# Kernel optimization log

Hardware: AMD Instinct MI355X
Metric: run time of the kernel (lower is better)

## Reference

```python
import jax, jax.numpy as jnp
import numpy as np

N, D_IN, D_OUT, N_CTRS, K = 16384, 64, 64, 512, 16


def setup_inputs() -> dict:
    key = jax.random.key(0)
    k1, k2, k3, k4 = jax.random.split(key, 4)
    x = jax.random.normal(k1, (N, D_IN), dtype=jnp.float32)
    ctrs = jax.random.normal(k2, (N_CTRS, D_IN), dtype=jnp.float32)
    Wv = jax.random.normal(k3, (N_CTRS, D_IN, D_OUT), dtype=jnp.float32) * 0.02
    Ov = jax.random.normal(k4, (N_CTRS, D_OUT), dtype=jnp.float32) * 0.02
    return {"x": x, "ctrs": ctrs, "Wv": Wv, "Ov": Ov, "k": K}


def reference(x, ctrs, Wv, Ov, k):
    n = x.shape[0]
    # squared distances via expansion (same math as sum((x-c)^2), avoids [n,C,d] blowup)
    x2 = jnp.sum(x * x, axis=1, keepdims=True)            # [n,1]
    c2 = jnp.sum(ctrs * ctrs, axis=1)                     # [C]
    dist_sq = x2 + c2[None, :] - 2.0 * (x @ ctrs.T)       # [n,C]
    # k nearest centers; softmax over negative squared distances of the k selected
    neg_top, idx = jax.lax.top_k(-dist_sq, k)             # [n,k] each
    scores = jax.nn.softmax(neg_top, axis=1)              # [n,k]
    # dense soft-assignment matrix (only k nonzeros per row), as in the torch code
    A = jnp.zeros_like(dist_sq).at[jnp.arange(n)[:, None], idx].set(scores)  # [n,C]
    # per-token affine mix: sum_c A[n,c] * (x[n] @ Wv[c] + Ov[c])
    scored_weights = jnp.einsum('nc,cgp->ngp', A, Wv)     # [n,d_in,d_out]
    out = jnp.einsum('ngp,ng->np', scored_weights, x) + A @ Ov  # [n,d_out]
    return out
```

## Files before the change

kernel.cpp:

```cpp
#include <hip/hip_runtime.h>
#include <hip/hip_fp16.h>

#define N_TOK 16384
#define D 64
#define NC 512
#define KSEL 16
#define NPAIR (N_TOK * KSEL)
#define PADCAP 327168

typedef __attribute__((ext_vector_type(8))) short short8;
typedef __attribute__((ext_vector_type(8))) unsigned short ushort8;
typedef __attribute__((ext_vector_type(16))) float float16;

__device__ __forceinline__ unsigned fkey(float f) {
    unsigned u = __float_as_uint(f);
    return (u & 0x80000000u) ? ~u : (u | 0x80000000u);
}
__device__ __forceinline__ float funkey(unsigned k) {
    unsigned u = (k & 0x80000000u) ? (k & 0x7fffffffu) : ~k;
    return __uint_as_float(u);
}
__device__ __forceinline__ unsigned short bfr(float f) {
    unsigned u = __float_as_uint(f);
    return (unsigned short)((u + 0x7FFFu + ((u >> 16) & 1u)) >> 16);
}
__device__ __forceinline__ float b2f(unsigned short h) {
    return __uint_as_float((unsigned)h << 16);
}

__device__ __forceinline__ void ins16(unsigned (&run)[16], unsigned k) {
    #pragma unroll
    for (int r = 0; r < 16; ++r) {
        unsigned mx = run[r] > k ? run[r] : k;
        unsigned mn = run[r] > k ? k : run[r];
        run[r] = mx; k = mn;
    }
}

__global__ __launch_bounds__(256) void prep_kernel(
    const float* __restrict__ x, const float* __restrict__ ctrs,
    unsigned short* __restrict__ xh, unsigned short* __restrict__ xl,
    unsigned short* __restrict__ cbf, float* __restrict__ c2g) {
    const int b = blockIdx.x, t = threadIdx.x;
    if (b < 512) {
        int g = b * 256 + t;
        int row = g >> 3, seg = g & 7;
        const float4* xp = (const float4*)(x + row * 64 + seg * 8);
        float4 u = xp[0], v = xp[1];
        float c[8] = {u.x, u.y, u.z, u.w, v.x, v.y, v.z, v.w};
        ushort8 h, l;
        #pragma unroll
        for (int j = 0; j < 8; ++j) {
            h[j] = bfr(c[j]);
            l[j] = bfr(c[j] - b2f(h[j]));
        }
        *(ushort8*)(xh + row * 64 + seg * 8) = h;
        *(ushort8*)(xl + row * 64 + seg * 8) = l;
    } else {
        int g = (b - 512) * 256 + t;
        int c = g >> 1, q = g & 1;
        const float4* cp = (const float4*)(ctrs + c * D + q * 32);
        unsigned short* Ch = cbf + c * 136 + q * 32;
        float s2 = 0.f;
        #pragma unroll
        for (int i = 0; i < 8; ++i) {
            float4 v = cp[i];
            s2 += v.x * v.x + v.y * v.y + v.z * v.z + v.w * v.w;
            unsigned short h0 = bfr(v.x), h1 = bfr(v.y), h2 = bfr(v.z), h3 = bfr(v.w);
            unsigned short l0 = bfr(v.x - b2f(h0)), l1 = bfr(v.y - b2f(h1));
            unsigned short l2 = bfr(v.z - b2f(h2)), l3 = bfr(v.w - b2f(h3));
            *(uint2*)(Ch + 4 * i) =
                make_uint2((unsigned)h0 | ((unsigned)h1 << 16),
                           (unsigned)h2 | ((unsigned)h3 << 16));
            *(uint2*)(Ch + 64 + 4 * i) =
                make_uint2((unsigned)l0 | ((unsigned)l1 << 16),
                           (unsigned)l2 | ((unsigned)l3 << 16));
        }
        s2 += __shfl_xor(s2, 1);
        c2g[c] = s2;
    }
}

__global__ __launch_bounds__(256, 4) void topk15_kernel(
    const unsigned short* __restrict__ xh, const unsigned short* __restrict__ xl,
    const unsigned short* __restrict__ cbf, const float* __restrict__ c2g,
    unsigned* __restrict__ pk) {
    __shared__ __align__(16) unsigned char pool[35328];
    unsigned short* Cbf = (unsigned short*)pool;
    unsigned* Sbk = (unsigned*)pool;
    unsigned* mbp = (unsigned*)pool;
    float* c2s = (float*)(pool + 34816);

    const int t = threadIdx.x;
    const int lane = t & 63;
    const int wv = t >> 6;
    const int mrow = lane & 31;
    const int half = lane >> 5;
    const int tb = blockIdx.x >> 2;
    const int p = blockIdx.x & 3;
    const int base = tb * 64;
    const int cbase = p * 128;
    const int trow = (wv & 1) * 32;
    const int cgrp = (wv >> 1) * 64;

    {
        const uint4* src = (const uint4*)(cbf + (size_t)cbase * 136);
        uint4* dst = (uint4*)pool;
        #pragma unroll
        for (int i = 0; i < 8; ++i) dst[t + 256 * i] = src[t + 256 * i];
        if (t < 128) {
            dst[2048 + t] = src[2048 + t];
            c2s[t] = c2g[cbase + t];
        }
    }

    short8 ah[4], al[4];
    {
        const int xrow = base + trow + mrow;
        const unsigned short* xph = xh + (size_t)xrow * 64 + half * 8;
        const unsigned short* xpl = xl + (size_t)xrow * 64 + half * 8;
        #pragma unroll
        for (int kt = 0; kt < 4; ++kt) {
            ah[kt] = *(const short8*)(xph + kt * 16);
            al[kt] = *(const short8*)(xpl + kt * 16);
        }
    }
    __syncthreads();

    float16 acc0 = {0.f,0.f,0.f,0.f,0.f,0.f,0.f,0.f,0.f,0.f,0.f,0.f,0.f,0.f,0.f,0.f};
    float16 acc1 = acc0;

    const unsigned short* B0 = Cbf + (cgrp + mrow) * 136 + half * 8;
    const unsigned short* B1 = Cbf + (cgrp + 32 + mrow) * 136 + half * 8;
    #pragma unroll
    for (int kt = 0; kt < 4; ++kt) {
        short8 bh0 = *(const short8*)(B0 + kt * 16);
        short8 bh1 = *(const short8*)(B1 + kt * 16);
        short8 bl0 = *(const short8*)(B0 + 64 + kt * 16);
        short8 bl1 = *(const short8*)(B1 + 64 + kt * 16);
        acc0 = __builtin_amdgcn_mfma_f32_32x32x16_bf16(ah[kt], bh0, acc0, 0, 0, 0);
        acc1 = __builtin_amdgcn_mfma_f32_32x32x16_bf16(ah[kt], bh1, acc1, 0, 0, 0);
        acc0 = __builtin_amdgcn_mfma_f32_32x32x16_bf16(al[kt], bh0, acc0, 0, 0, 0);
        acc1 = __builtin_amdgcn_mfma_f32_32x32x16_bf16(al[kt], bh1, acc1, 0, 0, 0);
        acc0 = __builtin_amdgcn_mfma_f32_32x32x16_bf16(ah[kt], bl0, acc0, 0, 0, 0);
        acc1 = __builtin_amdgcn_mfma_f32_32x32x16_bf16(ah[kt], bl1, acc1, 0, 0, 0);
    }
    __syncthreads();

    {
        float ca = c2s[cgrp + mrow];
        float cb = c2s[cgrp + 32 + mrow];
        #pragma unroll
        for (int reg = 0; reg < 16; ++reg) {
            int tokrow = trow + (reg & 3) + 8 * (reg >> 2) + 4 * half;
            float sa = fmaf(2.f, acc0[reg], -ca);
            float sb = fmaf(2.f, acc1[reg], -cb);
            Sbk[tokrow * 132 + cgrp + mrow] =
                (fkey(sa) & 0xFFFFFE00u) | (unsigned)(cbase + cgrp + mrow);
            Sbk[tokrow * 132 + cgrp + 32 + mrow] =
                (fkey(sb) & 0xFFFFFE00u) | (unsigned)(cbase + cgrp + 32 + mrow);
        }
    }
    __syncthreads();

    const int tok = t & 63;
    const int h = t >> 6;
    unsigned run[16];
    #pragma unroll
    for (int r = 0; r < 16; ++r) run[r] = 0u;
    #pragma unroll
    for (int i = 0; i < 8; ++i) {
        int cq = ((i + tok) & 7) ^ ((tok >> 3) & 7);
        uint4 kv = *(const uint4*)(Sbk + tok * 132 + 32 * h + 4 * cq);
        ins16(run, kv.x); ins16(run, kv.y); ins16(run, kv.z); ins16(run, kv.w);
    }
    __syncthreads();

    {
        uint4* dst = (uint4*)(mbp + tok * 68 + h * 16);
        dst[0] = make_uint4(run[0], run[1], run[2], run[3]);
        dst[1] = make_uint4(run[4], run[5], run[6], run[7]);
        dst[2] = make_uint4(run[8], run[9], run[10], run[11]);
        dst[3] = make_uint4(run[12], run[13], run[14], run[15]);
    }
    __syncthreads();

    if (t < 64) {
        const unsigned* pm = mbp + t * 68;
        unsigned hv[4]; int pos[4];
        #pragma unroll
        for (int w = 0; w < 4; ++w) { pos[w] = 0; hv[w] = pm[w * 16]; }
        unsigned mm[16];
        #pragma unroll
        for (int r = 0; r < 16; ++r) {
            unsigned m = hv[0];
            #pragma unroll
            for (int w = 1; w < 4; ++w) m = m > hv[w] ? m : hv[w];
            mm[r] = m;
            #pragma unroll
            for (int w = 0; w < 4; ++w) {
                if (hv[w] == m) {
                    ++pos[w];
                    hv[w] = (pos[w] < 16) ? pm[w * 16 + pos[w]] : 0u;
                }
            }
        }
        uint4* dst = (uint4*)(pk + (size_t)(base + t) * 64 + p * 16);
        dst[0] = make_uint4(mm[0], mm[1], mm[2], mm[3]);
        dst[1] = make_uint4(mm[4], mm[5], mm[6], mm[7]);
        dst[2] = make_uint4(mm[8], mm[9], mm[10], mm[11]);
        dst[3] = make_uint4(mm[12], mm[13], mm[14], mm[15]);
    }
}

__global__ __launch_bounds__(256) void topmerge_kernel(
    const unsigned* __restrict__ pk, float* __restrict__ scores,
    int* __restrict__ sidx, int* __restrict__ hist) {
    __shared__ int lhist[NC];
    const int t = threadIdx.x;
    lhist[t] = 0; lhist[t + 256] = 0;
    __syncthreads();
    const int n = blockIdx.x * 256 + t;
    const unsigned* p = pk + (size_t)n * 64;
    unsigned h[4]; int pos[4];
    #pragma unroll
    for (int w = 0; w < 4; ++w) { pos[w] = 0; h[w] = p[w * 16]; }
    float vals[16]; int ids[16];
    #pragma unroll
    for (int r = 0; r < KSEL; ++r) {
        unsigned m = h[0];
        #pragma unroll
        for (int w = 1; w < 4; ++w) m = m > h[w] ? m : h[w];
        vals[r] = funkey(m);
        ids[r] = (int)(m & 511u);
        #pragma unroll
        for (int w = 0; w < 4; ++w) {
            if (h[w] == m) {
                ++pos[w];
                h[w] = (pos[w] < KSEL) ? p[w * 16 + pos[w]] : 0u;
            }
        }
    }
    float mx = vals[0];
    float e[16]; float sum = 0.f;
    #pragma unroll
    for (int r = 0; r < KSEL; ++r) { e[r] = __expf(vals[r] - mx); sum += e[r]; }
    float inv = 1.f / sum;
    #pragma unroll
    for (int q = 0; q < 4; ++q) {
        *(float4*)(scores + n * KSEL + 4 * q) =
            make_float4(e[4*q] * inv, e[4*q+1] * inv, e[4*q+2] * inv, e[4*q+3] * inv);
        *(int4*)(sidx + n * KSEL + 4 * q) =
            make_int4(ids[4*q], ids[4*q+1], ids[4*q+2], ids[4*q+3]);
    }
    #pragma unroll
    for (int r = 0; r < KSEL; ++r) atomicAdd(&lhist[ids[r]], 1);
    __syncthreads();
    { int hv = lhist[t]; if (hv) atomicAdd(&hist[t], hv); }
    { int hv = lhist[t + 256]; if (hv) atomicAdd(&hist[t + 256], hv); }
}

__global__ __launch_bounds__(256) void scatter5_kernel(
    const int* __restrict__ hist, const int* __restrict__ sidx,
    const float* __restrict__ scores, int* __restrict__ cursor,
    int* __restrict__ tokentab, float* __restrict__ scotab,
    int* __restrict__ meta) {
    __shared__ int buf[2][NC];
    __shared__ int sb[NC];
    __shared__ int lh[NC];
    __shared__ int lbase[NC];
    const int t = threadIdx.x;

    int h0 = hist[t], h1 = hist[t + 256];
    int p0 = (h0 + 127) & ~127, p1 = (h1 + 127) & ~127;
    buf[0][t] = p0; buf[0][t + 256] = p1;
    __syncthreads();
    int a = 0;
    for (int d = 1; d < NC; d <<= 1) {
        int v0 = buf[a][t] + (t >= d ? buf[a][t - d] : 0);
        int v1 = buf[a][t + 256] + (t + 256 >= d ? buf[a][t + 256 - d] : 0);
        buf[1 - a][t] = v0; buf[1 - a][t + 256] = v1;
        __syncthreads();
        a ^= 1;
    }
    sb[t] = buf[a][t] - p0;
    sb[t + 256] = buf[a][t + 256] - p1;
    if (t == 255) meta[0] = buf[a][NC - 1];
    lh[t] = 0; lh[t + 256] = 0;
    __syncthreads();

    const int base_e = blockIdx.x * 1024;
    int myc[4];
    #pragma unroll
    for (int i = 0; i < 4; ++i) {
        int c = sidx[base_e + t + 256 * i];
        myc[i] = c;
        atomicAdd(&lh[c], 1);
    }
    __syncthreads();
    for (int i = t; i < NC; i += 256) {
        int h = lh[i];
        lbase[i] = h ? (sb[i] + atomicAdd(&cursor[i], h)) : 0;
        lh[i] = 0;
    }
    __syncthreads();
    #pragma unroll
    for (int i = 0; i < 4; ++i) {
        int e = base_e + t + 256 * i;
        int c = myc[i];
        int pos = lbase[c] + atomicAdd(&lh[c], 1);
        tokentab[pos] = (c << 19) | e;
        scotab[pos] = scores[e];
    }
}

__global__ __launch_bounds__(256) void mix16_kernel(
    const float* __restrict__ x, const float* __restrict__ Wv,
    const float* __restrict__ Ov, const int* __restrict__ tokentab,
    const float* __restrict__ scotab, const int* __restrict__ meta,
    __half* __restrict__ partial) {
    __shared__ __align__(16) unsigned short Wt[64 * 72];
    __shared__ int eT[128];
    __shared__ float sT[128];

    const int t = threadIdx.x;
    const int base = blockIdx.x * 128;
    if (base >= meta[0]) return;

    const int c = (int)(((unsigned)tokentab[base]) >> 19);

    {
        const float* Wp = Wv + c * (D * D) + (t & 63);
        const int gb = (t >> 6) * 16;
        #pragma unroll
        for (int g = 0; g < 16; g += 2) {
            float v0 = Wp[(gb + g) * 64];
            float v1 = Wp[(gb + g + 1) * 64];
            unsigned pkw = (unsigned)bfr(v0) | ((unsigned)bfr(v1) << 16);
            *(unsigned*)&Wt[(t & 63) * 72 + gb + g] = pkw;
        }
    }
    if (t < 128) {
        unsigned w = (unsigned)tokentab[base + t];
        eT[t] = (int)(w & 0x7FFFFu);
        sT[t] = scotab[base + t];
    }
    __syncthreads();

    const int lane = t & 63;
    const int wv = t >> 6;
    const int mrow = lane & 31;
    const int half = lane >> 5;
    const int row = wv * 32 + mrow;

    const int   mye = eT[row];
    const int   myn = (mye < NPAIR) ? (mye >> 4) : 0;
    const float mys = sT[row];

    const float* xp = x + myn * D + half * 8;
    float4 f[8];
    #pragma unroll
    for (int kt = 0; kt < 4; ++kt) {
        f[2 * kt]     = *(const float4*)(xp + kt * 16);
        f[2 * kt + 1] = *(const float4*)(xp + kt * 16 + 4);
    }
    short8 a[4];
    #pragma unroll
    for (int kt = 0; kt < 4; ++kt) {
        float4 u = f[2 * kt], v = f[2 * kt + 1];
        a[kt][0] = (short)bfr(u.x * mys); a[kt][1] = (short)bfr(u.y * mys);
        a[kt][2] = (short)bfr(u.z * mys); a[kt][3] = (short)bfr(u.w * mys);
        a[kt][4] = (short)bfr(v.x * mys); a[kt][5] = (short)bfr(v.y * mys);
        a[kt][6] = (short)bfr(v.z * mys); a[kt][7] = (short)bfr(v.w * mys);
    }

    float16 acc0 = {0.f,0.f,0.f,0.f,0.f,0.f,0.f,0.f,0.f,0.f,0.f,0.f,0.f,0.f,0.f,0.f};
    float16 acc1 = {0.f,0.f,0.f,0.f,0.f,0.f,0.f,0.f,0.f,0.f,0.f,0.f,0.f,0.f,0.f,0.f};

    const unsigned short* B0 = Wt + mrow * 72;
    const unsigned short* B1 = Wt + (mrow + 32) * 72;
    #pragma unroll
    for (int kt = 0; kt < 4; ++kt) {
        short8 b0 = *(const short8*)(B0 + kt * 16 + half * 8);
        short8 b1 = *(const short8*)(B1 + kt * 16 + half * 8);
        acc0 = __builtin_amdgcn_mfma_f32_32x32x16_bf16(a[kt], b0, acc0, 0, 0, 0);
        acc1 = __builtin_amdgcn_mfma_f32_32x32x16_bf16(a[kt], b1, acc1, 0, 0, 0);
    }

    const float ov0 = Ov[c * D + mrow];
    const float ov1 = Ov[c * D + 32 + mrow];
    #pragma unroll
    for (int reg = 0; reg < 16; ++reg) {
        int orow = wv * 32 + (reg & 3) + 8 * (reg >> 2) + 4 * half;
        float s = sT[orow];
        int e = eT[orow];
        if (e < NPAIR) {
            __half* dst = partial + (size_t)e * D;
            dst[mrow]      = __float2half(acc0[reg] + s * ov0);
            dst[32 + mrow] = __float2half(acc1[reg] + s * ov1);
        }
    }
}

__global__ __launch_bounds__(256) void redu2_kernel(
    const __half* __restrict__ partial, float* __restrict__ out) {
    const int g = blockIdx.x * 256 + threadIdx.x;
    const int n = g >> 3;
    const int d8 = (g & 7) * 8;
    const __half* p = partial + (size_t)n * (KSEL * D) + d8;
    float s[8] = {0.f, 0.f, 0.f, 0.f, 0.f, 0.f, 0.f, 0.f};
    #pragma unroll
    for (int r = 0; r < KSEL; ++r) {
        ushort8 v = *(const ushort8*)(p + r * D);
        #pragma unroll
        for (int j = 0; j < 8; ++j)
            s[j] += __half2float(__ushort_as_half((unsigned short)v[j]));
    }
    float* o = out + n * D + d8;
    *(float4*)(o)     = make_float4(s[0], s[1], s[2], s[3]);
    *(float4*)(o + 4) = make_float4(s[4], s[5], s[6], s[7]);
}

__global__ __launch_bounds__(256) void mix14_kernel(
    const float* __restrict__ x, const float* __restrict__ Wv,
    const float* __restrict__ Ov, const int* __restrict__ tokentab,
    const float* __restrict__ scotab, const int* __restrict__ meta,
    float* __restrict__ out) {
    __shared__ __align__(16) unsigned short Wt[64 * 72];
    __shared__ int tT[128];
    __shared__ float sT[128];

    const int t = threadIdx.x;
    const int base = blockIdx.x * 128;
    if (base >= meta[0]) return;

    const int c = (int)(((unsigned)tokentab[base]) >> 19);

    {
        const float* Wp = Wv + c * (D * D) + (t & 63);
        const int gb = (t >> 6) * 16;
        #pragma unroll
        for (int g = 0; g < 16; g += 2) {
            float v0 = Wp[(gb + g) * 64];
            float v1 = Wp[(gb + g + 1) * 64];
            unsigned pkw = (unsigned)bfr(v0) | ((unsigned)bfr(v1) << 16);
            *(unsigned*)&Wt[(t & 63) * 72 + gb + g] = pkw;
        }
    }
    if (t < 128) {
        unsigned w = (unsigned)tokentab[base + t];
        tT[t] = (int)((w & 0x7FFFFu) >> 4);
        sT[t] = scotab[base + t];
    }
    __syncthreads();

    const int lane = t & 63;
    const int wv = t >> 6;
    const int mrow = lane & 31;
    const int half = lane >> 5;
    const int row = wv * 32 + mrow;

    const int   myn = tT[row];
    const float mys = sT[row];

    const float* xp = x + myn * D + half * 8;
    float4 f[8];
    #pragma unroll
    for (int kt = 0; kt < 4; ++kt) {
        f[2 * kt]     = *(const float4*)(xp + kt * 16);
        f[2 * kt + 1] = *(const float4*)(xp + kt * 16 + 4);
    }
    short8 a[4];
    #pragma unroll
    for (int kt = 0; kt < 4; ++kt) {
        float4 u = f[2 * kt], v = f[2 * kt + 1];
        a[kt][0] = (short)bfr(u.x * mys); a[kt][1] = (short)bfr(u.y * mys);
        a[kt][2] = (short)bfr(u.z * mys); a[kt][3] = (short)bfr(u.w * mys);
        a[kt][4] = (short)bfr(v.x * mys); a[kt][5] = (short)bfr(v.y * mys);
        a[kt][6] = (short)bfr(v.z * mys); a[kt][7] = (short)bfr(v.w * mys);
    }

    float16 acc0 = {0.f,0.f,0.f,0.f,0.f,0.f,0.f,0.f,0.f,0.f,0.f,0.f,0.f,0.f,0.f,0.f};
    float16 acc1 = {0.f,0.f,0.f,0.f,0.f,0.f,0.f,0.f,0.f,0.f,0.f,0.f,0.f,0.f,0.f,0.f};

    const unsigned short* B0 = Wt + mrow * 72;
    const unsigned short* B1 = Wt + (mrow + 32) * 72;
    #pragma unroll
    for (int kt = 0; kt < 4; ++kt) {
        short8 b0 = *(const short8*)(B0 + kt * 16 + half * 8);
        short8 b1 = *(const short8*)(B1 + kt * 16 + half * 8);
        acc0 = __builtin_amdgcn_mfma_f32_32x32x16_bf16(a[kt], b0, acc0, 0, 0, 0);
        acc1 = __builtin_amdgcn_mfma_f32_32x32x16_bf16(a[kt], b1, acc1, 0, 0, 0);
    }

    const float ov0 = Ov[c * D + mrow];
    const float ov1 = Ov[c * D + 32 + mrow];
    #pragma unroll
    for (int reg = 0; reg < 16; ++reg) {
        int orow = wv * 32 + (reg & 3) + 8 * (reg >> 2) + 4 * half;
        float s = sT[orow];
        if (s != 0.f) {
            int n = tT[orow];
            unsafeAtomicAdd(out + n * D + mrow,      acc0[reg] + s * ov0);
            unsafeAtomicAdd(out + n * D + 32 + mrow, acc1[reg] + s * ov1);
        }
    }
}

extern "C" void kernel_launch(void* const* d_in, const int* in_sizes, int n_in,
                              void* d_out, int out_size, void* d_ws, size_t ws_size,
                              hipStream_t stream) {
    const float* x    = (const float*)d_in[0];
    const float* ctrs = (const float*)d_in[1];
    const float* Wv   = (const float*)d_in[2];
    const float* Ov   = (const float*)d_in[3];
    float* out = (float*)d_out;

    const size_t OFF_META = 0;
    const size_t OFF_HIST = 512;
    const size_t OFF_CUR  = 1024;
    const size_t OFF_SCO  = 2560;
    const size_t OFF_SIDX = OFF_SCO + NPAIR;
    const size_t OFF_TTAB = OFF_SIDX + NPAIR;
    const size_t OFF_STAB = OFF_TTAB + PADCAP;
    const size_t OFF_PK   = OFF_STAB + PADCAP;
    const size_t OFF_XH   = OFF_PK + (size_t)N_TOK * 16;
    const size_t PK_INTS  = (size_t)N_TOK * 64;
    const size_t XH_INTS  = (size_t)N_TOK * 32;
    const size_t CBF_INTS = (size_t)NC * 68;
    const size_t O_PK   = OFF_STAB + PADCAP;
    const size_t O_XH   = O_PK + PK_INTS;
    const size_t O_XL   = O_XH + XH_INTS;
    const size_t O_CBF  = O_XL + XH_INTS;
    const size_t O_C2   = O_CBF + CBF_INTS;
    const size_t O_PART = O_C2 + 512;
    const size_t PART_INTS = (size_t)NPAIR * 32;

    int*    meta     = (int*)d_ws + OFF_META;
    int*    hist     = (int*)d_ws + OFF_HIST;
    int*    cursor   = (int*)d_ws + OFF_CUR;
    float*  scores   = (float*)d_ws + OFF_SCO;
    int*    sidx     = (int*)d_ws + OFF_SIDX;
    int*    tokentab = (int*)d_ws + OFF_TTAB;
    float*  scotab   = (float*)d_ws + OFF_STAB;
    unsigned* pkbuf  = (unsigned*)((int*)d_ws + O_PK);
    unsigned short* xh  = (unsigned short*)((int*)d_ws + O_XH);
    unsigned short* xl  = (unsigned short*)((int*)d_ws + O_XL);
    unsigned short* cbf = (unsigned short*)((int*)d_ws + O_CBF);
    float*  c2g      = (float*)((int*)d_ws + O_C2);
    __half* partial  = (__half*)((int*)d_ws + O_PART);

    const size_t need = (O_PART + PART_INTS) * 4;
    const bool fast = ws_size >= need;

    hipMemsetAsync(hist, 0, 2 * NC * sizeof(int), stream);
    if (fast) {
        hipMemsetAsync(tokentab, 0xFF, (size_t)PADCAP * sizeof(int), stream);
    } else {
        hipMemsetAsync(out, 0, (size_t)N_TOK * D * sizeof(float), stream);
        hipMemsetAsync(scotab, 0, (size_t)PADCAP * sizeof(float), stream);
        hipMemsetAsync(tokentab, 0, (size_t)PADCAP * sizeof(int), stream);
    }
    hipLaunchKernelGGL(prep_kernel, dim3(516), dim3(256), 0, stream,
                       x, ctrs, xh, xl, cbf, c2g);
    hipLaunchKernelGGL(topk15_kernel, dim3((N_TOK / 64) * 4), dim3(256), 0, stream,
                       xh, xl, cbf, c2g, pkbuf);
    hipLaunchKernelGGL(topmerge_kernel, dim3(N_TOK / 256), dim3(256), 0, stream,
                       pkbuf, scores, sidx, hist);
    hipLaunchKernelGGL(scatter5_kernel, dim3(256), dim3(256), 0, stream,
                       hist, sidx, scores, cursor, tokentab, scotab, meta);
    if (fast) {
        hipLaunchKernelGGL(mix16_kernel, dim3(PADCAP / 128), dim3(256), 0, stream,
                           x, Wv, Ov, tokentab, scotab, meta, partial);
        hipLaunchKernelGGL(redu2_kernel, dim3(N_TOK * 8 / 256), dim3(256), 0, stream,
                           partial, out);
    } else {
        hipLaunchKernelGGL(mix14_kernel, dim3(PADCAP / 128), dim3(256), 0, stream,
                           x, Wv, Ov, tokentab, scotab, meta, out);
    }
}
```

Measured before the change: 143.3 us.

## Pretranspose Wv to bf16 in prep kernel and fold memsets into it

```diff
diff --git a/kernel.cpp b/kernel.cpp
--- a/kernel.cpp
+++ b/kernel.cpp
@@ -37,10 +37,14 @@
     }
 }
 
-__global__ __launch_bounds__(256) void prep_kernel(
+__global__ __launch_bounds__(256) void prep2_kernel(
     const float* __restrict__ x, const float* __restrict__ ctrs,
+    const float* __restrict__ Wv,
     unsigned short* __restrict__ xh, unsigned short* __restrict__ xl,
-    unsigned short* __restrict__ cbf, float* __restrict__ c2g) {
+    unsigned short* __restrict__ cbf, float* __restrict__ c2g,
+    unsigned short* __restrict__ wbt, int* __restrict__ tokentab,
+    int* __restrict__ hist) {
+    __shared__ unsigned short tw[64 * 68];
     const int b = blockIdx.x, t = threadIdx.x;
     if (b < 512) {
         int g = b * 256 + t;
@@ -56,7 +60,7 @@
         }
         *(ushort8*)(xh + row * 64 + seg * 8) = h;
         *(ushort8*)(xl + row * 64 + seg * 8) = l;
-    } else {
+    } else if (b < 516) {
         int g = (b - 512) * 256 + t;
         int c = g >> 1, q = g & 1;
         const float4* cp = (const float4*)(ctrs + c * D + q * 32);
@@ -78,6 +82,29 @@
         }
         s2 += __shfl_xor(s2, 1);
         c2g[c] = s2;
+    } else if (b < 1028) {
+        const float* Wp = Wv + (size_t)(b - 516) * 4096;
+        #pragma unroll
+        for (int i = 0; i < 16; ++i) {
+            int e = t + 256 * i;
+            tw[(e & 63) * 68 + (e >> 6)] = bfr(Wp[e]);
+        }
+        __syncthreads();
+        unsigned short* Wo = wbt + (size_t)(b - 516) * 4096;
+        #pragma unroll
+        for (int i = 0; i < 2; ++i) {
+            int idx8 = t + 256 * i;
+            int p = idx8 >> 3, g0 = (idx8 & 7) * 8;
+            ushort8 v;
+            #pragma unroll
+            for (int j = 0; j < 8; ++j) v[j] = tw[p * 68 + g0 + j];
+            *(ushort8*)(Wo + idx8 * 8) = v;
+        }
+    } else if (b < 1348) {
+        int i = (b - 1028) * 256 + t;
+        if (i < PADCAP / 4) ((int4*)tokentab)[i] = make_int4(-1, -1, -1, -1);
+    } else {
+        hist[t] = 0; hist[t + 256] = 0; hist[t + 512] = 0; hist[t + 768] = 0;
     }
 }
 
@@ -314,8 +341,8 @@
     }
 }
 
-__global__ __launch_bounds__(256) void mix16_kernel(
-    const float* __restrict__ x, const float* __restrict__ Wv,
+__global__ __launch_bounds__(256) void mix17_kernel(
+    const unsigned short* __restrict__ xh, const unsigned short* __restrict__ wbt,
     const float* __restrict__ Ov, const int* __restrict__ tokentab,
     const float* __restrict__ scotab, const int* __restrict__ meta,
     __half* __restrict__ partial) {
@@ -330,15 +357,12 @@
     const int c = (int)(((unsigned)tokentab[base]) >> 19);
 
     {
-        const float* Wp = Wv + c * (D * D) + (t & 63);
-        const int gb = (t >> 6) * 16;
-        #pragma unroll
-        for (int g = 0; g < 16; g += 2) {
-            float v0 = Wp[(gb + g) * 64];
-            float v1 = Wp[(gb + g + 1) * 64];
-            unsigned pkw = (unsigned)bfr(v0) | ((unsigned)bfr(v1) << 16);
-            *(unsigned*)&Wt[(t & 63) * 72 + gb + g] = pkw;
-        }
+        const unsigned short* Wp = wbt + (size_t)c * 4096;
+        const int p = t >> 2, qq = t & 3;
+        *(ushort8*)(Wt + p * 72 + qq * 16) =
+            *(const ushort8*)(Wp + p * 64 + qq * 16);
+        *(ushort8*)(Wt + p * 72 + qq * 16 + 8) =
+            *(const ushort8*)(Wp + p * 64 + qq * 16 + 8);
     }
     if (t < 128) {
         unsigned w = (unsigned)tokentab[base + t];
@@ -353,26 +377,13 @@
     const int half = lane >> 5;
     const int row = wv * 32 + mrow;
 
-    const int   mye = eT[row];
-    const int   myn = (mye < NPAIR) ? (mye >> 4) : 0;
-    const float mys = sT[row];
-
-    const float* xp = x + myn * D + half * 8;
-    float4 f[8];
-    #pragma unroll
-    for (int kt = 0; kt < 4; ++kt) {
-        f[2 * kt]     = *(const float4*)(xp + kt * 16);
-        f[2 * kt + 1] = *(const float4*)(xp + kt * 16 + 4);
-    }
+    const int mye = eT[row];
+    const int myn = (mye < NPAIR) ? (mye >> 4) : 0;
+
+    const unsigned short* xp = xh + (size_t)myn * 64 + half * 8;
     short8 a[4];
     #pragma unroll
-    for (int kt = 0; kt < 4; ++kt) {
-        float4 u = f[2 * kt], v = f[2 * kt + 1];
-        a[kt][0] = (short)bfr(u.x * mys); a[kt][1] = (short)bfr(u.y * mys);
-        a[kt][2] = (short)bfr(u.z * mys); a[kt][3] = (short)bfr(u.w * mys);
-        a[kt][4] = (short)bfr(v.x * mys); a[kt][5] = (short)bfr(v.y * mys);
-        a[kt][6] = (short)bfr(v.z * mys); a[kt][7] = (short)bfr(v.w * mys);
-    }
+    for (int kt = 0; kt < 4; ++kt) a[kt] = *(const short8*)(xp + kt * 16);
 
     float16 acc0 = {0.f,0.f,0.f,0.f,0.f,0.f,0.f,0.f,0.f,0.f,0.f,0.f,0.f,0.f,0.f,0.f};
     float16 acc1 = {0.f,0.f,0.f,0.f,0.f,0.f,0.f,0.f,0.f,0.f,0.f,0.f,0.f,0.f,0.f,0.f};
@@ -396,8 +407,8 @@
         int e = eT[orow];
         if (e < NPAIR) {
             __half* dst = partial + (size_t)e * D;
-            dst[mrow]      = __float2half(acc0[reg] + s * ov0);
-            dst[32 + mrow] = __float2half(acc1[reg] + s * ov1);
+            dst[mrow]      = __float2half(s * (acc0[reg] + ov0));
+            dst[32 + mrow] = __float2half(s * (acc1[reg] + ov1));
         }
     }
 }
@@ -523,17 +534,17 @@
     const size_t OFF_SIDX = OFF_SCO + NPAIR;
     const size_t OFF_TTAB = OFF_SIDX + NPAIR;
     const size_t OFF_STAB = OFF_TTAB + PADCAP;
-    const size_t OFF_PK   = OFF_STAB + PADCAP;
-    const size_t OFF_XH   = OFF_PK + (size_t)N_TOK * 16;
     const size_t PK_INTS  = (size_t)N_TOK * 64;
     const size_t XH_INTS  = (size_t)N_TOK * 32;
     const size_t CBF_INTS = (size_t)NC * 68;
+    const size_t WBT_INTS = (size_t)NC * 2048;
     const size_t O_PK   = OFF_STAB + PADCAP;
     const size_t O_XH   = O_PK + PK_INTS;
     const size_t O_XL   = O_XH + XH_INTS;
     const size_t O_CBF  = O_XL + XH_INTS;
     const size_t O_C2   = O_CBF + CBF_INTS;
-    const size_t O_PART = O_C2 + 512;
+    const size_t O_WBT  = O_C2 + 512;
+    const size_t O_PART = O_WBT + WBT_INTS;
     const size_t PART_INTS = (size_t)NPAIR * 32;
 
     int*    meta     = (int*)d_ws + OFF_META;
@@ -548,21 +559,19 @@
     unsigned short* xl  = (unsigned short*)((int*)d_ws + O_XL);
     unsigned short* cbf = (unsigned short*)((int*)d_ws + O_CBF);
     float*  c2g      = (float*)((int*)d_ws + O_C2);
+    unsigned short* wbt = (unsigned short*)((int*)d_ws + O_WBT);
     __half* partial  = (__half*)((int*)d_ws + O_PART);
 
     const size_t need = (O_PART + PART_INTS) * 4;
     const bool fast = ws_size >= need;
 
-    hipMemsetAsync(hist, 0, 2 * NC * sizeof(int), stream);
-    if (fast) {
-        hipMemsetAsync(tokentab, 0xFF, (size_t)PADCAP * sizeof(int), stream);
-    } else {
+    hipLaunchKernelGGL(prep2_kernel, dim3(1349), dim3(256), 0, stream,
+                       x, ctrs, Wv, xh, xl, cbf, c2g, wbt, tokentab, hist);
+    if (!fast) {
         hipMemsetAsync(out, 0, (size_t)N_TOK * D * sizeof(float), stream);
         hipMemsetAsync(scotab, 0, (size_t)PADCAP * sizeof(float), stream);
         hipMemsetAsync(tokentab, 0, (size_t)PADCAP * sizeof(int), stream);
     }
-    hipLaunchKernelGGL(prep_kernel, dim3(516), dim3(256), 0, stream,
-                       x, ctrs, xh, xl, cbf, c2g);
     hipLaunchKernelGGL(topk15_kernel, dim3((N_TOK / 64) * 4), dim3(256), 0, stream,
                        xh, xl, cbf, c2g, pkbuf);
     hipLaunchKernelGGL(topmerge_kernel, dim3(N_TOK / 256), dim3(256), 0, stream,
@@ -570,8 +579,8 @@
     hipLaunchKernelGGL(scatter5_kernel, dim3(256), dim3(256), 0, stream,
                        hist, sidx, scores, cursor, tokentab, scotab, meta);
     if (fast) {
-        hipLaunchKernelGGL(mix16_kernel, dim3(PADCAP / 128), dim3(256), 0, stream,
-                           x, Wv, Ov, tokentab, scotab, meta, partial);
+        hipLaunchKernelGGL(mix17_kernel, dim3(PADCAP / 128), dim3(256), 0, stream,
+                           xh, wbt, Ov, tokentab, scotab, meta, partial);
         hipLaunchKernelGGL(redu2_kernel, dim3(N_TOK * 8 / 256), dim3(256), 0, stream,
                            partial, out);
     } else {
```

Result: faster. 134.2 us, median of 2 (-6.4%).
